# Kernel tuning notes

Hardware: AMD Instinct MI355X
Metric: run time of the kernel (lower is better)

The kernel has to match this reference:

```python
import jax, jax.numpy as jnp
import numpy as np
from jax import lax

N_WORDS = 8192
MAX_WLEN = 16
VOCAB = 500
EMB = 64
HID = 256
N_SENT = 256
SENT_LEN = 32  # N_SENT * SENT_LEN == N_WORDS (sentlens are uniform)


def setup_inputs() -> dict:
    key = jax.random.key(0)
    ks = jax.random.split(key, 12)
    chars = jax.random.randint(ks[0], (N_WORDS, MAX_WLEN), 1, VOCAB, dtype=jnp.int32)
    # packed LSTM requires lengths sorted descending
    wordlens = jnp.sort(jax.random.randint(ks[1], (N_WORDS,), 1, MAX_WLEN + 1, dtype=jnp.int32))[::-1]
    # permutation mapping sorted order -> original order (tensor_unsort input)
    word_orig_idx = jax.random.permutation(ks[2], N_WORDS).astype(jnp.int32)
    emb_table = (jax.random.normal(ks[3], (VOCAB, EMB), dtype=jnp.float32) * 0.1).at[0].set(0.0)  # padding_idx=0
    W_ih = jax.random.normal(ks[4], (4 * HID, EMB), dtype=jnp.float32) * 0.05
    W_hh = jax.random.normal(ks[5], (4 * HID, HID), dtype=jnp.float32) * 0.05
    b_ih = jax.random.normal(ks[6], (4 * HID,), dtype=jnp.float32) * 0.02
    b_hh = jax.random.normal(ks[7], (4 * HID,), dtype=jnp.float32) * 0.02
    attn_w = jax.random.normal(ks[8], (HID,), dtype=jnp.float32) * 0.1  # char_attn weight (zero-init in orig; random for nontrivial test)
    h_init = jax.random.normal(ks[9], (HID,), dtype=jnp.float32) * 0.02  # charlstm_h_init (num_layers=1)
    c_init = jax.random.normal(ks[10], (HID,), dtype=jnp.float32) * 0.02
    return dict(chars=chars, wordlens=wordlens, word_orig_idx=word_orig_idx,
                emb_table=emb_table, W_ih=W_ih, W_hh=W_hh, b_ih=b_ih, b_hh=b_hh,
                attn_w=attn_w, h_init=h_init, c_init=c_init)


def _char_model(chars, wordlens, word_orig_idx, emb_table, W_ih, W_hh, b_ih, b_hh, attn_w, h_init, c_init):
    n = chars.shape[0]
    pad_mask = jnp.arange(MAX_WLEN)[None, :] >= wordlens[:, None]  # [N,L] True where padded
    embs = emb_table[chars]  # [N,L,E] (dropout is identity at eval)

    def step(carry, x_t):
        h, c = carry
        gates = x_t @ W_ih.T + h @ W_hh.T + (b_ih + b_hh)  # [N,4H]
        i, f, g, o = jnp.split(gates, 4, axis=-1)  # torch gate order i,f,g,o
        c = jax.nn.sigmoid(f) * c + jax.nn.sigmoid(i) * jnp.tanh(g)
        h = jax.nn.sigmoid(o) * jnp.tanh(c)
        return (h, c), h

    h0 = jnp.broadcast_to(h_init, (n, HID))
    c0 = jnp.broadcast_to(c_init, (n, HID))
    _, hs = lax.scan(step, (h0, c0), embs.transpose(1, 0, 2))  # hs: [L,N,H]
    char_reps = hs.transpose(1, 0, 2)  # [N,L,H]
    # pad_packed_sequence yields zeros at padded positions
    char_reps = jnp.where(pad_mask[..., None], 0.0, char_reps)
    # masked sigmoid attention pool: weights.bmm(char_reps)
    w = jax.nn.sigmoid(char_reps @ attn_w)  # [N,L]
    w = jnp.where(pad_mask, 0.0, w)
    res = jnp.einsum('nl,nlh->nh', w, char_reps)  # [N,H]
    # tensor_unsort: restore original word order
    res = jnp.zeros_like(res).at[word_orig_idx].set(res)
    # split(sentlens) + pack + pad_packed with uniform sentlens -> reshape
    return res.reshape(N_SENT, SENT_LEN, HID)


def reference(chars, wordlens, word_orig_idx, emb_table, W_ih, W_hh, b_ih, b_hh, attn_w, h_init, c_init):
    return _char_model(chars, wordlens, word_orig_idx, emb_table, W_ih, W_hh, b_ih, b_hh, attn_w, h_init, c_init)
```

## Files before the change

### kernel.cpp

```cpp
#include <hip/hip_runtime.h>
#include <math.h>

#define HID 256
#define EMB 64
#define KTOT 320
#define MT 32
#define NBLK 256
#define THREADS 512
#define KT 10
#define KT_STREAM 6
#define KT_RES 4
#define XSTR 328

typedef _Float16 f16;
typedef _Float16 f16x4 __attribute__((ext_vector_type(4)));
typedef _Float16 f16x8 __attribute__((ext_vector_type(8)));
typedef float f32x4 __attribute__((ext_vector_type(4)));

__device__ __forceinline__ float sigm(float x) { return 1.0f / (1.0f + __expf(-x)); }
__device__ __forceinline__ float tanh_fast(float x) {
  return 1.0f - 2.0f / (__expf(2.0f * x) + 1.0f);
}

__global__ __launch_bounds__(KTOT) void prep_w(const float* __restrict__ W_ih,
                                               const float* __restrict__ W_hh,
                                               const float* __restrict__ b_ih,
                                               const float* __restrict__ b_hh,
                                               f16* __restrict__ Wfrag,
                                               float* __restrict__ bias_p) {
  const int g = blockIdx.x;
  const int k = threadIdx.x;
  const int q = g >> 8, u = g & 255;
  const int col = ((u >> 5) << 7) + (q << 5) + (((u >> 4) & 1) << 4) + (u & 15);
  const float w = (k < HID) ? W_hh[g * HID + k] : W_ih[g * EMB + (k - HID)];
  const int kt = k >> 5;
  Wfrag[((size_t)(kt * 1024 + col)) * 32 + (k & 31)] = (f16)w;
  if (k == 0) bias_p[col] = b_ih[g] + b_hh[g];
}

__global__ __launch_bounds__(THREADS, 2) void lstm_mfma(
    const int* __restrict__ chars, const int* __restrict__ wordlens,
    const int* __restrict__ orig_idx, const float* __restrict__ emb_table,
    const float* __restrict__ attn_w, const float* __restrict__ h_init,
    const float* __restrict__ c_init, const f16* __restrict__ Wfrag,
    const float* __restrict__ bias_p, float* __restrict__ out) {
  __shared__ __align__(16) f16 Xs[MT * XSTR];
  __shared__ __align__(16) float attP[MT * 8];
  __shared__ int chars_s[MT * 16];
  __shared__ int len_s[MT];
  __shared__ int oidx_s[MT];

  const int tid  = threadIdx.x;
  const int w0   = blockIdx.x * MT;
  const int lane = tid & 63;
  const int wv   = tid >> 6;
  const int r15  = lane & 15, c4 = lane >> 4;
  const int u0   = wv * 32 + r15;

  chars_s[tid] = chars[w0 * 16 + tid];
  if (tid < MT) { len_s[tid] = wordlens[w0 + tid]; oidx_s[tid] = orig_idx[w0 + tid]; }

  {
    const int j = tid & 255, mb = tid >> 8;
    const f16 hv = (f16)h_init[j];
#pragma unroll
    for (int mm = 0; mm < 16; ++mm) Xs[(mb + mm * 2) * XSTR + j] = hv;
  }
  {
    const int m = tid >> 4, e4 = tid & 15;
    const int ch_g = chars[(w0 + m) * 16 + 0];
    const float4 e = ((const float4*)emb_table)[ch_g * 16 + e4];
    f16x4 ev = { (f16)e.x, (f16)e.y, (f16)e.z, (f16)e.w };
    *(f16x4*)&Xs[m * XSTR + HID + e4 * 4] = ev;
  }

  const float aw0 = attn_w[u0];
  const float aw1 = attn_w[u0 + 16];
  float biasr[4][2];
#pragma unroll
  for (int q = 0; q < 4; ++q) {
    biasr[q][0] = bias_p[wv * 128 + q * 32 + r15];
    biasr[q][1] = bias_p[wv * 128 + q * 32 + 16 + r15];
  }

  float c_reg[2][8], res[2][8], h_new[2][8];
  {
    const float c0 = c_init[u0], c1 = c_init[u0 + 16];
#pragma unroll
    for (int i = 0; i < 8; ++i) {
      c_reg[0][i] = c0; c_reg[1][i] = c1;
      res[0][i] = 0.0f; res[1][i] = 0.0f;
      h_new[0][i] = 0.0f; h_new[1][i] = 0.0f;
    }
  }

  const size_t bofs = (size_t)(wv * 128 + r15) * 4 + c4;

  f16x8 Wr[KT_RES][8];
#pragma unroll
  for (int kt = 0; kt < KT_RES; ++kt) {
    const f16x8* __restrict__ Wp = ((const f16x8*)Wfrag) + (size_t)(kt + KT_STREAM) * 4096;
#pragma unroll
    for (int f = 0; f < 8; ++f) Wr[kt][f] = Wp[bofs + (size_t)f * 64];
  }

  __syncthreads();

  int steps = 1;
#pragma unroll
  for (int m = 0; m < MT; ++m) steps = max(steps, len_s[m]);
  int lenr[8];
#pragma unroll
  for (int mt = 0; mt < 2; ++mt)
#pragma unroll
    for (int r = 0; r < 4; ++r) lenr[mt * 4 + r] = len_s[mt * 16 + c4 * 4 + r];

  for (int t = 0; t < steps; ++t) {
    f32x4 acc[4][2][2];
#pragma unroll
    for (int q = 0; q < 4; ++q)
#pragma unroll
      for (int s = 0; s < 2; ++s) {
        const float b = biasr[q][s];
        const f32x4 b4 = { b, b, b, b };
        acc[q][s][0] = b4; acc[q][s][1] = b4;
      }

#pragma unroll 2
    for (int kt = 0; kt < KT_STREAM; ++kt) {
      const f16x8* __restrict__ Wp = ((const f16x8*)Wfrag) + (size_t)kt * 4096;
      f16x8 bb[8];
#pragma unroll
      for (int f = 0; f < 8; ++f) bb[f] = Wp[bofs + (size_t)f * 64];
      const f16x8 a0 = *(const f16x8*)&Xs[r15 * XSTR + kt * 32 + c4 * 8];
      const f16x8 a1 = *(const f16x8*)&Xs[(16 + r15) * XSTR + kt * 32 + c4 * 8];
#pragma unroll
      for (int q = 0; q < 4; ++q)
#pragma unroll
        for (int s = 0; s < 2; ++s) {
          acc[q][s][0] = __builtin_amdgcn_mfma_f32_16x16x32_f16(a0, bb[q * 2 + s], acc[q][s][0], 0, 0, 0);
          acc[q][s][1] = __builtin_amdgcn_mfma_f32_16x16x32_f16(a1, bb[q * 2 + s], acc[q][s][1], 0, 0, 0);
        }
    }

#pragma unroll
    for (int kt = 0; kt < KT_RES; ++kt) {
      const int kk = kt + KT_STREAM;
      const f16x8 a0 = *(const f16x8*)&Xs[r15 * XSTR + kk * 32 + c4 * 8];
      const f16x8 a1 = *(const f16x8*)&Xs[(16 + r15) * XSTR + kk * 32 + c4 * 8];
#pragma unroll
      for (int q = 0; q < 4; ++q)
#pragma unroll
        for (int s = 0; s < 2; ++s) {
          acc[q][s][0] = __builtin_amdgcn_mfma_f32_16x16x32_f16(a0, Wr[kt][q * 2 + s], acc[q][s][0], 0, 0, 0);
          acc[q][s][1] = __builtin_amdgcn_mfma_f32_16x16x32_f16(a1, Wr[kt][q * 2 + s], acc[q][s][1], 0, 0, 0);
        }
    }

#pragma unroll
    for (int s = 0; s < 2; ++s)
#pragma unroll
      for (int mt = 0; mt < 2; ++mt)
#pragma unroll
        for (int r = 0; r < 4; ++r) {
          const int i = mt * 4 + r;
          const float gi = acc[0][s][mt][r];
          const float gf = acc[1][s][mt][r];
          const float gg = acc[2][s][mt][r];
          const float go = acc[3][s][mt][r];
          const float cc = sigm(gf) * c_reg[s][i] + sigm(gi) * tanh_fast(gg);
          c_reg[s][i] = cc;
          h_new[s][i] = sigm(go) * tanh_fast(cc);
        }

    __syncthreads();

    if (t + 1 < steps) {
#pragma unroll
      for (int s = 0; s < 2; ++s)
#pragma unroll
        for (int mt = 0; mt < 2; ++mt)
#pragma unroll
          for (int r = 0; r < 4; ++r)
            Xs[(mt * 16 + c4 * 4 + r) * XSTR + u0 + s * 16] = (f16)h_new[s][mt * 4 + r];
      {
        const int m = tid >> 4, e4 = tid & 15;
        const int ch = chars_s[m * 16 + (t + 1)];
        const float4 e = ((const float4*)emb_table)[ch * 16 + e4];
        f16x4 ev = { (f16)e.x, (f16)e.y, (f16)e.z, (f16)e.w };
        *(f16x4*)&Xs[m * XSTR + HID + e4 * 4] = ev;
      }
    }

#pragma unroll
    for (int mt = 0; mt < 2; ++mt)
#pragma unroll
      for (int r = 0; r < 4; ++r) {
        const int i = mt * 4 + r;
        float p = h_new[0][i] * aw0 + h_new[1][i] * aw1;
        p += __shfl_xor(p, 1); p += __shfl_xor(p, 2);
        p += __shfl_xor(p, 4); p += __shfl_xor(p, 8);
        if (r15 == 0) attP[(mt * 16 + c4 * 4 + r) * 8 + wv] = p;
      }

    __syncthreads();

#pragma unroll
    for (int mt = 0; mt < 2; ++mt)
#pragma unroll
      for (int r = 0; r < 4; ++r) {
        const int i = mt * 4 + r;
        const int w = mt * 16 + c4 * 4 + r;
        const f32x4 p0 = *(const f32x4*)&attP[w * 8];
        const f32x4 p1 = *(const f32x4*)&attP[w * 8 + 4];
        const float sum = (p0[0] + p0[1]) + (p0[2] + p0[3]) + (p1[0] + p1[1]) + (p1[2] + p1[3]);
        const float wgt = (t < lenr[i]) ? sigm(sum) : 0.0f;
        res[0][i] = fmaf(wgt, h_new[0][i], res[0][i]);
        res[1][i] = fmaf(wgt, h_new[1][i], res[1][i]);
      }
  }

#pragma unroll
  for (int s = 0; s < 2; ++s)
#pragma unroll
    for (int mt = 0; mt < 2; ++mt)
#pragma unroll
      for (int r = 0; r < 4; ++r) {
        const int w = mt * 16 + c4 * 4 + r;
        out[(size_t)oidx_s[w] * HID + u0 + s * 16] = res[s][mt * 4 + r];
      }
}

extern "C" void kernel_launch(void* const* d_in, const int* in_sizes, int n_in,
                              void* d_out, int out_size, void* d_ws, size_t ws_size,
                              hipStream_t stream) {
  const int*   chars    = (const int*)d_in[0];
  const int*   wordlens = (const int*)d_in[1];
  const int*   orig_idx = (const int*)d_in[2];
  const float* emb      = (const float*)d_in[3];
  const float* W_ih     = (const float*)d_in[4];
  const float* W_hh     = (const float*)d_in[5];
  const float* b_ih     = (const float*)d_in[6];
  const float* b_hh     = (const float*)d_in[7];
  const float* attn_w   = (const float*)d_in[8];
  const float* h_init   = (const float*)d_in[9];
  const float* c_init   = (const float*)d_in[10];
  float* out = (float*)d_out;

  f16*   Wfrag  = (f16*)d_ws;
  float* bias_p = (float*)((char*)d_ws + (size_t)KTOT * 1024 * sizeof(f16));
  if (ws_size < (size_t)KTOT * 1024 * sizeof(f16) + 1024 * sizeof(float)) return;

  hipLaunchKernelGGL(prep_w, dim3(1024), dim3(KTOT), 0, stream,
                     W_ih, W_hh, b_ih, b_hh, Wfrag, bias_p);
  hipLaunchKernelGGL(lstm_mfma, dim3(NBLK), dim3(THREADS), 0, stream,
                     chars, wordlens, orig_idx, emb, attn_w, h_init, c_init,
                     Wfrag, bias_p, out);
}
```

Before: 260.2 us.

## Double-buffer LDS state to drop one barrier per step; stream all weights

Double-buffers the hidden-state/embedding tile and the attention partials in LDS, so each step needs one __syncthreads instead of two. The attention-weight accumulation for step t is deferred to the start of step t+1, with a final epilogue after the loop. It also removes the register-resident copy of the last 4 weight k-tiles and streams all 10 tiles from global/L2 every step. That frees registers but adds extra global loads per step, and the LDS footprint doubles.

```diff
diff --git a/kernel.cpp b/kernel.cpp
--- a/kernel.cpp
+++ b/kernel.cpp
@@ -8,8 +8,6 @@
 #define NBLK 256
 #define THREADS 512
 #define KT 10
-#define KT_STREAM 6
-#define KT_RES 4
 #define XSTR 328
 
 typedef _Float16 f16;
@@ -44,8 +42,8 @@
     const float* __restrict__ attn_w, const float* __restrict__ h_init,
     const float* __restrict__ c_init, const f16* __restrict__ Wfrag,
     const float* __restrict__ bias_p, float* __restrict__ out) {
-  __shared__ __align__(16) f16 Xs[MT * XSTR];
-  __shared__ __align__(16) float attP[MT * 8];
+  __shared__ __align__(16) f16 Xs[2][MT * XSTR];
+  __shared__ __align__(16) float attP[2][MT * 8];
   __shared__ int chars_s[MT * 16];
   __shared__ int len_s[MT];
   __shared__ int oidx_s[MT];
@@ -64,14 +62,14 @@
     const int j = tid & 255, mb = tid >> 8;
     const f16 hv = (f16)h_init[j];
 #pragma unroll
-    for (int mm = 0; mm < 16; ++mm) Xs[(mb + mm * 2) * XSTR + j] = hv;
+    for (int mm = 0; mm < 16; ++mm) Xs[0][(mb + mm * 2) * XSTR + j] = hv;
   }
   {
     const int m = tid >> 4, e4 = tid & 15;
     const int ch_g = chars[(w0 + m) * 16 + 0];
     const float4 e = ((const float4*)emb_table)[ch_g * 16 + e4];
     f16x4 ev = { (f16)e.x, (f16)e.y, (f16)e.z, (f16)e.w };
-    *(f16x4*)&Xs[m * XSTR + HID + e4 * 4] = ev;
+    *(f16x4*)&Xs[0][m * XSTR + HID + e4 * 4] = ev;
   }
 
   const float aw0 = attn_w[u0];
@@ -94,16 +92,6 @@
     }
   }
 
-  const size_t bofs = (size_t)(wv * 128 + r15) * 4 + c4;
-
-  f16x8 Wr[KT_RES][8];
-#pragma unroll
-  for (int kt = 0; kt < KT_RES; ++kt) {
-    const f16x8* __restrict__ Wp = ((const f16x8*)Wfrag) + (size_t)(kt + KT_STREAM) * 4096;
-#pragma unroll
-    for (int f = 0; f < 8; ++f) Wr[kt][f] = Wp[bofs + (size_t)f * 64];
-  }
-
   __syncthreads();
 
   int steps = 1;
@@ -115,7 +103,30 @@
 #pragma unroll
     for (int r = 0; r < 4; ++r) lenr[mt * 4 + r] = len_s[mt * 16 + c4 * 4 + r];
 
+  const size_t bofs = (size_t)(wv * 128 + r15) * 4 + c4;
+
   for (int t = 0; t < steps; ++t) {
+    const int cur = t & 1;
+    const f16* __restrict__ Xr = &Xs[cur][0];
+    f16* __restrict__ Xw = &Xs[cur ^ 1][0];
+
+    if (t > 0) {
+      const float* __restrict__ aP = &attP[cur ^ 1][0];
+#pragma unroll
+      for (int mt = 0; mt < 2; ++mt)
+#pragma unroll
+        for (int r = 0; r < 4; ++r) {
+          const int i = mt * 4 + r;
+          const int w = mt * 16 + c4 * 4 + r;
+          const f32x4 p0 = *(const f32x4*)&aP[w * 8];
+          const f32x4 p1 = *(const f32x4*)&aP[w * 8 + 4];
+          const float sum = (p0[0] + p0[1]) + (p0[2] + p0[3]) + (p1[0] + p1[1]) + (p1[2] + p1[3]);
+          const float wgt = (t - 1 < lenr[i]) ? sigm(sum) : 0.0f;
+          res[0][i] = fmaf(wgt, h_new[0][i], res[0][i]);
+          res[1][i] = fmaf(wgt, h_new[1][i], res[1][i]);
+        }
+    }
+
     f32x4 acc[4][2][2];
 #pragma unroll
     for (int q = 0; q < 4; ++q)
@@ -127,33 +138,19 @@
       }
 
 #pragma unroll 2
-    for (int kt = 0; kt < KT_STREAM; ++kt) {
+    for (int kt = 0; kt < KT; ++kt) {
       const f16x8* __restrict__ Wp = ((const f16x8*)Wfrag) + (size_t)kt * 4096;
       f16x8 bb[8];
 #pragma unroll
       for (int f = 0; f < 8; ++f) bb[f] = Wp[bofs + (size_t)f * 64];
-      const f16x8 a0 = *(const f16x8*)&Xs[r15 * XSTR + kt * 32 + c4 * 8];
-      const f16x8 a1 = *(const f16x8*)&Xs[(16 + r15) * XSTR + kt * 32 + c4 * 8];
+      const f16x8 a0 = *(const f16x8*)&Xr[r15 * XSTR + kt * 32 + c4 * 8];
+      const f16x8 a1 = *(const f16x8*)&Xr[(16 + r15) * XSTR + kt * 32 + c4 * 8];
 #pragma unroll
       for (int q = 0; q < 4; ++q)
 #pragma unroll
         for (int s = 0; s < 2; ++s) {
           acc[q][s][0] = __builtin_amdgcn_mfma_f32_16x16x32_f16(a0, bb[q * 2 + s], acc[q][s][0], 0, 0, 0);
           acc[q][s][1] = __builtin_amdgcn_mfma_f32_16x16x32_f16(a1, bb[q * 2 + s], acc[q][s][1], 0, 0, 0);
-        }
-    }
-
-#pragma unroll
-    for (int kt = 0; kt < KT_RES; ++kt) {
-      const int kk = kt + KT_STREAM;
-      const f16x8 a0 = *(const f16x8*)&Xs[r15 * XSTR + kk * 32 + c4 * 8];
-      const f16x8 a1 = *(const f16x8*)&Xs[(16 + r15) * XSTR + kk * 32 + c4 * 8];
-#pragma unroll
-      for (int q = 0; q < 4; ++q)
-#pragma unroll
-        for (int s = 0; s < 2; ++s) {
-          acc[q][s][0] = __builtin_amdgcn_mfma_f32_16x16x32_f16(a0, Wr[kt][q * 2 + s], acc[q][s][0], 0, 0, 0);
-          acc[q][s][1] = __builtin_amdgcn_mfma_f32_16x16x32_f16(a1, Wr[kt][q * 2 + s], acc[q][s][1], 0, 0, 0);
         }
     }
 
@@ -173,8 +170,6 @@
           h_new[s][i] = sigm(go) * tanh_fast(cc);
         }
 
-    __syncthreads();
-
     if (t + 1 < steps) {
 #pragma unroll
       for (int s = 0; s < 2; ++s)
@@ -182,39 +177,45 @@
         for (int mt = 0; mt < 2; ++mt)
 #pragma unroll
           for (int r = 0; r < 4; ++r)
-            Xs[(mt * 16 + c4 * 4 + r) * XSTR + u0 + s * 16] = (f16)h_new[s][mt * 4 + r];
+            Xw[(mt * 16 + c4 * 4 + r) * XSTR + u0 + s * 16] = (f16)h_new[s][mt * 4 + r];
       {
         const int m = tid >> 4, e4 = tid & 15;
         const int ch = chars_s[m * 16 + (t + 1)];
         const float4 e = ((const float4*)emb_table)[ch * 16 + e4];
         f16x4 ev = { (f16)e.x, (f16)e.y, (f16)e.z, (f16)e.w };
-        *(f16x4*)&Xs[m * XSTR + HID + e4 * 4] = ev;
-      }
-    }
-
-#pragma unroll
-    for (int mt = 0; mt < 2; ++mt)
-#pragma unroll
-      for (int r = 0; r < 4; ++r) {
-        const int i = mt * 4 + r;
-        float p = h_new[0][i] * aw0 + h_new[1][i] * aw1;
-        p += __shfl_xor(p, 1); p += __shfl_xor(p, 2);
-        p += __shfl_xor(p, 4); p += __shfl_xor(p, 8);
-        if (r15 == 0) attP[(mt * 16 + c4 * 4 + r) * 8 + wv] = p;
-      }
+        *(f16x4*)&Xw[m * XSTR + HID + e4 * 4] = ev;
+      }
+    }
+
+    {
+      float* __restrict__ aW = &attP[cur][0];
+#pragma unroll
+      for (int mt = 0; mt < 2; ++mt)
+#pragma unroll
+        for (int r = 0; r < 4; ++r) {
+          const int i = mt * 4 + r;
+          float p = h_new[0][i] * aw0 + h_new[1][i] * aw1;
+          p += __shfl_xor(p, 1); p += __shfl_xor(p, 2);
+          p += __shfl_xor(p, 4); p += __shfl_xor(p, 8);
+          if (r15 == 0) aW[(mt * 16 + c4 * 4 + r) * 8 + wv] = p;
+        }
+    }
 
     __syncthreads();
-
+  }
+
+  {
+    const float* __restrict__ aP = &attP[(steps - 1) & 1][0];
 #pragma unroll
     for (int mt = 0; mt < 2; ++mt)
 #pragma unroll
       for (int r = 0; r < 4; ++r) {
         const int i = mt * 4 + r;
         const int w = mt * 16 + c4 * 4 + r;
-        const f32x4 p0 = *(const f32x4*)&attP[w * 8];
-        const f32x4 p1 = *(const f32x4*)&attP[w * 8 + 4];
+        const f32x4 p0 = *(const f32x4*)&aP[w * 8];
+        const f32x4 p1 = *(const f32x4*)&aP[w * 8 + 4];
         const float sum = (p0[0] + p0[1]) + (p0[2] + p0[3]) + (p1[0] + p1[1]) + (p1[2] + p1[3]);
-        const float wgt = (t < lenr[i]) ? sigm(sum) : 0.0f;
+        const float wgt = (steps - 1 < lenr[i]) ? sigm(sum) : 0.0f;
         res[0][i] = fmaf(wgt, h_new[0][i], res[0][i]);
         res[1][i] = fmaf(wgt, h_new[1][i], res[1][i]);
       }
```

Result: no change. 261.4 us (+0.5%).
